# Optimization experiments

Measured on AMD Instinct MI355X. Metric: run time of the kernel, lower is better.

## Reference

```python
import jax, jax.numpy as jnp
import numpy as np

D_MODEL = 1024
N_HEADS = 16
D_K = D_MODEL // N_HEADS


def setup_inputs() -> dict:
    key = jax.random.key(0)
    ks = jax.random.split(key, 9)
    s = 1.0 / np.sqrt(D_MODEL)
    inp = {
        "x": jax.random.normal(ks[0], (2, 2048, D_MODEL), dtype=jnp.float32),
        "wq": jax.random.uniform(ks[1], (D_MODEL, D_MODEL), jnp.float32, -s, s),
        "bq": jax.random.uniform(ks[2], (D_MODEL,), jnp.float32, -s, s),
        "wk": jax.random.uniform(ks[3], (D_MODEL, D_MODEL), jnp.float32, -s, s),
        "bk": jax.random.uniform(ks[4], (D_MODEL,), jnp.float32, -s, s),
        "wv": jax.random.uniform(ks[5], (D_MODEL, D_MODEL), jnp.float32, -s, s),
        "bv": jax.random.uniform(ks[6], (D_MODEL,), jnp.float32, -s, s),
        "wo": jax.random.uniform(ks[7], (D_MODEL, D_MODEL), jnp.float32, -s, s),
        "bo": jax.random.uniform(ks[8], (D_MODEL,), jnp.float32, -s, s),
    }
    return inp


def reference(x, wq, bq, wk, bk, wv, bv, wo, bo):
    B, S, _ = x.shape
    # projections; weights stored as [in, out] (torch Linear applies x @ W^T; here W pre-transposed)
    def proj(w, b):
        y = x @ w + b  # [B,S,D]
        return y.reshape(B, S, N_HEADS, D_K).transpose(0, 2, 1, 3)  # [B,H,S,dk]
    q, k, v = proj(wq, bq), proj(wk, bk), proj(wv, bv)
    scores = jnp.einsum('bhqd,bhkd->bhqk', q, k) / jnp.sqrt(jnp.float32(D_K))
    attn = jax.nn.softmax(scores, axis=-1)  # dropout p=0 -> identity
    ctx = jnp.einsum('bhqk,bhkd->bhqd', attn, v)
    ctx = ctx.transpose(0, 2, 1, 3).reshape(B, S, D_MODEL)
    return ctx @ wo + bo
```

## Files before the change

kernel.cpp:

```cpp
#include <hip/hip_runtime.h>
#include <hip/hip_bf16.h>
#include <math.h>


typedef __attribute__((ext_vector_type(8))) short bf8v;
typedef __attribute__((ext_vector_type(4))) float f32x4;
typedef __attribute__((ext_vector_type(16))) float f32x16;

#define mfma32(a, b, c) __builtin_amdgcn_mfma_f32_32x32x16_bf16((a), (b), (c), 0, 0, 0)

constexpr int Dm = 1024;
constexpr int NH = 16;
constexpr int DK = 64;
constexpr int BB = 2;
constexpr int SS = 2048;
constexpr int MM = BB * SS;

__device__ __forceinline__ unsigned short f2bf(float f) {
  union { float f; unsigned u; } v; v.f = f;
  unsigned r = v.u + 0x7fffu + ((v.u >> 16) & 1u);
  return (unsigned short)(r >> 16);
}

__device__ __forceinline__ unsigned cvt_pk_bf16(float lo, float hi) {
  unsigned r;
  asm("v_cvt_pk_bf16_f32 %0, %1, %2" : "=v"(r) : "v"(lo), "v"(hi));
  return r;
}

__device__ __forceinline__ void swap32(unsigned &a, unsigned &b) {
  asm("v_permlane32_swap_b32 %0, %1" : "+v"(a), "+v"(b));
}

__device__ __forceinline__ void gl_lds16(const void* g, void* l) {
  __builtin_amdgcn_global_load_lds(
      (const __attribute__((address_space(1))) void*)g,
      (__attribute__((address_space(3))) void*)l, 16, 0, 0);
}

__device__ __forceinline__ int swz4(int r) { return (r ^ (r >> 2)) & 3; }
__device__ __forceinline__ bf8v frag4(const unsigned short* base, int R, int s0) {
  return *(const bf8v*)((const char*)base + R * 64 + ((s0 ^ swz4(R)) << 4));
}
__device__ __forceinline__ bf8v rd8(const unsigned short* base, int row, int slot) {
  return *(const bf8v*)((const char*)base + row * 128 + (((slot ^ row) & 7) << 4));
}

__global__ __launch_bounds__(256) void transw_kernel(
    const float* __restrict__ w0, const float* __restrict__ w1,
    const float* __restrict__ w2, const float* __restrict__ w3,
    unsigned short* __restrict__ dstBase)
{
  const float* src = (blockIdx.y == 0) ? w0 : (blockIdx.y == 1) ? w1
                   : (blockIdx.y == 2) ? w2 : w3;
  unsigned short* dst = dstBase + (size_t)blockIdx.y * (Dm * Dm);
  int idx = blockIdx.x * 256 + threadIdx.x;
  int i = idx & (Dm - 1);
  int o = (idx >> 10) << 2;
  float4 v = *(const float4*)(src + (size_t)i * Dm + o);
  dst[(size_t)(o + 0) * Dm + i] = f2bf(v.x);
  dst[(size_t)(o + 1) * Dm + i] = f2bf(v.y);
  dst[(size_t)(o + 2) * Dm + i] = f2bf(v.z);
  dst[(size_t)(o + 3) * Dm + i] = f2bf(v.w);
}

__global__ __launch_bounds__(256) void xconv_kernel(
    const float* __restrict__ x, unsigned short* __restrict__ xb)
{
  int idx = blockIdx.x * 256 + threadIdx.x;
  const float* s = x + (size_t)idx * 8;
  float4 a = *(const float4*)s;
  float4 b = *(const float4*)(s + 4);
  union { bf8v v; unsigned w[4]; } u;
  u.w[0] = cvt_pk_bf16(a.x, a.y); u.w[1] = cvt_pk_bf16(a.z, a.w);
  u.w[2] = cvt_pk_bf16(b.x, b.y); u.w[3] = cvt_pk_bf16(b.z, b.w);
  *(bf8v*)(xb + (size_t)idx * 8) = u.v;
}

__global__ __launch_bounds__(256) void proj_kernel(
    const unsigned short* __restrict__ Xb, const unsigned short* __restrict__ WtBase,
    const float* __restrict__ bq, const float* __restrict__ bk, const float* __restrict__ bv,
    unsigned short* __restrict__ Qh, unsigned short* __restrict__ Kh,
    unsigned short* __restrict__ Vh)
{
  __shared__ unsigned short As[2][128 * 32];
  __shared__ unsigned short Bs[2][128 * 32];
  const int z = blockIdx.z;
  const unsigned short* W = WtBase + (size_t)z * (Dm * Dm);
  const float* bias = (z == 0) ? bq : (z == 1) ? bk : bv;

  const int tid = threadIdx.x, lane = tid & 63, wave = tid >> 6;
  const int wm = wave >> 1, wn = wave & 1;
  const int m0 = blockIdx.x * 128, n0 = blockIdx.y * 128;
  const int l15 = lane & 15, l4 = lane >> 4;

  const int q1 = tid, q2 = tid + 256;
  const int rw1 = q1 >> 2, sl1 = q1 & 3, c1 = sl1 ^ swz4(rw1);
  const int rw2 = q2 >> 2, sl2 = q2 & 3, c2 = sl2 ^ swz4(rw2);
  const int ldsOff1 = (q1 - lane) * 16, ldsOff2 = (q2 - lane) * 16;

  auto stageAB = [&](int buf, int k0) {
    gl_lds16(Xb + (size_t)(m0 + rw1) * Dm + k0 + c1 * 8, (char*)As[buf] + ldsOff1);
    gl_lds16(Xb + (size_t)(m0 + rw2) * Dm + k0 + c2 * 8, (char*)As[buf] + ldsOff2);
    gl_lds16(W + (size_t)(n0 + rw1) * Dm + k0 + c1 * 8, (char*)Bs[buf] + ldsOff1);
    gl_lds16(W + (size_t)(n0 + rw2) * Dm + k0 + c2 * 8, (char*)Bs[buf] + ldsOff2);
  };

  f32x4 acc[4][4] = {};

  stageAB(0, 0);
  __syncthreads();

  for (int k0 = 0; k0 < Dm; k0 += 32) {
    const int cur = (k0 >> 5) & 1, nxt = cur ^ 1;
    if (k0 + 32 < Dm) stageAB(nxt, k0 + 32);

    bf8v af[4], bfr[4];
    #pragma unroll
    for (int i = 0; i < 4; ++i) af[i] = frag4(As[cur], wm * 64 + i * 16 + l15, l4);
    #pragma unroll
    for (int j = 0; j < 4; ++j) bfr[j] = frag4(Bs[cur], wn * 64 + j * 16 + l15, l4);
    __builtin_amdgcn_s_setprio(1);
    #pragma unroll
    for (int i = 0; i < 4; ++i)
      #pragma unroll
      for (int j = 0; j < 4; ++j)
        acc[i][j] = __builtin_amdgcn_mfma_f32_16x16x32_bf16(af[i], bfr[j], acc[i][j], 0, 0, 0);
    __builtin_amdgcn_s_setprio(0);
    __syncthreads();
  }

  unsigned short* Out = (z == 0) ? Qh : (z == 1) ? Kh : Vh;
  const float oscale = (z == 0) ? 0.18033688011112042f : 1.0f;
  #pragma unroll
  for (int i = 0; i < 4; ++i)
    #pragma unroll
    for (int j = 0; j < 4; ++j) {
      int row = m0 + wm * 64 + i * 16 + l4 * 4;
      int col = n0 + wn * 64 + j * 16 + l15;
      float bcol = bias[col];
      int h = col >> 6, d = col & 63;
      #pragma unroll
      for (int r = 0; r < 4; ++r) {
        int rr = row + r;
        int b = rr >> 11, s = rr & 2047;
        unsigned short val = f2bf((acc[i][j][r] + bcol) * oscale);
        if (z < 2)
          Out[(((size_t)(b * NH + h) * SS + s) * DK) + d] = val;
        else
          Out[((size_t)(b * NH + h) * DK + d) * SS + s] = val;
      }
    }
}

__global__ __launch_bounds__(256) void outproj_kernel(
    const unsigned short* __restrict__ Ctx, const unsigned short* __restrict__ Wto,
    const float* __restrict__ bo, float* __restrict__ Out)
{
  __shared__ unsigned short As[2][128 * 32];
  __shared__ unsigned short Bs[2][128 * 32];
  const int tid = threadIdx.x, lane = tid & 63, wave = tid >> 6;
  const int wm = wave >> 1, wn = wave & 1;
  const int m0 = blockIdx.x * 128, n0 = blockIdx.y * 128;
  const int l15 = lane & 15, l4 = lane >> 4;

  const int q1 = tid, q2 = tid + 256;
  const int rw1 = q1 >> 2, sl1 = q1 & 3, c1 = sl1 ^ swz4(rw1);
  const int rw2 = q2 >> 2, sl2 = q2 & 3, c2 = sl2 ^ swz4(rw2);
  const int ldsOff1 = (q1 - lane) * 16, ldsOff2 = (q2 - lane) * 16;

  auto srcA = [&](int rw, int c, int k0) -> const unsigned short* {
    int rr = m0 + rw, b = rr >> 11, s = rr & 2047;
    int col = k0 + c * 8, h = col >> 6, d = col & 63;
    return Ctx + ((size_t)(b * NH + h) * SS + s) * DK + d;
  };
  auto stageAB = [&](int buf, int k0) {
    gl_lds16(srcA(rw1, c1, k0), (char*)As[buf] + ldsOff1);
    gl_lds16(srcA(rw2, c2, k0), (char*)As[buf] + ldsOff2);
    gl_lds16(Wto + (size_t)(n0 + rw1) * Dm + k0 + c1 * 8, (char*)Bs[buf] + ldsOff1);
    gl_lds16(Wto + (size_t)(n0 + rw2) * Dm + k0 + c2 * 8, (char*)Bs[buf] + ldsOff2);
  };

  f32x4 acc[4][4] = {};

  stageAB(0, 0);
  __syncthreads();

  for (int k0 = 0; k0 < Dm; k0 += 32) {
    const int cur = (k0 >> 5) & 1, nxt = cur ^ 1;
    if (k0 + 32 < Dm) stageAB(nxt, k0 + 32);

    bf8v af[4], bfr[4];
    #pragma unroll
    for (int i = 0; i < 4; ++i) af[i] = frag4(As[cur], wm * 64 + i * 16 + l15, l4);
    #pragma unroll
    for (int j = 0; j < 4; ++j) bfr[j] = frag4(Bs[cur], wn * 64 + j * 16 + l15, l4);
    __builtin_amdgcn_s_setprio(1);
    #pragma unroll
    for (int i = 0; i < 4; ++i)
      #pragma unroll
      for (int j = 0; j < 4; ++j)
        acc[i][j] = __builtin_amdgcn_mfma_f32_16x16x32_bf16(af[i], bfr[j], acc[i][j], 0, 0, 0);
    __builtin_amdgcn_s_setprio(0);
    __syncthreads();
  }

  #pragma unroll
  for (int i = 0; i < 4; ++i)
    #pragma unroll
    for (int j = 0; j < 4; ++j) {
      int row = m0 + wm * 64 + i * 16 + l4 * 4;
      int col = n0 + wn * 64 + j * 16 + l15;
      float bcol = bo[col];
      #pragma unroll
      for (int r = 0; r < 4; ++r)
        Out[(size_t)(row + r) * Dm + col] = acc[i][j][r] + bcol;
    }
}

__global__ __launch_bounds__(512, 4) void attn_kernel(
    const unsigned short* __restrict__ Q, const unsigned short* __restrict__ K,
    const unsigned short* __restrict__ Vt, unsigned short* __restrict__ CtxQ)
{
  __shared__ __align__(16) unsigned short smem[32768];
  unsigned short* KlB = smem;
  unsigned short* VlB = smem + 16384;

  const int tid = threadIdx.x, lane = tid & 63, wave = tid >> 6;
  const int qsub = wave & 3, khalf = wave >> 2;
  const int l31 = lane & 31, hi = lane >> 5;
  const int bh = blockIdx.y;
  const int q0 = blockIdx.x * 128 + qsub * 32;
  const size_t base = (size_t)bh * SS * DK;

  bf8v qf[4];
  #pragma unroll
  for (int dc = 0; dc < 4; ++dc)
    qf[dc] = *(const bf8v*)(Q + base + (size_t)(q0 + l31) * DK + dc * 16 + hi * 8);

  bf8v onesv;
  #pragma unroll
  for (int e = 0; e < 8; ++e) onesv[e] = (short)0x3F80;

  f32x16 cacc[2] = {};
  f32x16 lacc = {};

  const int srow = tid >> 3, ssl = tid & 7, sc = ssl ^ (srow & 7);
  const int soff = (tid - lane) * 16;
  auto kslab = [&](int buf, int h) { return KlB + (buf * 2 + h) * 4096; };
  auto vslab = [&](int buf, int h) { return VlB + (buf * 2 + h) * 4096; };
  auto stage = [&](int buf, int kt) {
    gl_lds16(K + base + (size_t)(kt + srow) * DK + sc * 8,          (char*)kslab(buf, 0) + soff);
    gl_lds16(K + base + (size_t)(1024 + kt + srow) * DK + sc * 8,   (char*)kslab(buf, 1) + soff);
    gl_lds16(Vt + base + (size_t)srow * SS + kt + sc * 8,           (char*)vslab(buf, 0) + soff);
    gl_lds16(Vt + base + (size_t)srow * SS + 1024 + kt + sc * 8,    (char*)vslab(buf, 1) + soff);
  };

  constexpr int NT = 16;
  stage(0, 0);
  __syncthreads();

  for (int t = 0; t < NT; ++t) {
    const int cur = t & 1;
    if (t + 1 < NT) stage(cur ^ 1, (t + 1) * 64);
    const unsigned short* Kb = kslab(cur, khalf);
    const unsigned short* Vb = vslab(cur, khalf);

    f32x16 st0 = {}, st1 = {};
    __builtin_amdgcn_s_setprio(1);
    #pragma unroll
    for (int dc = 0; dc < 4; ++dc) {
      bf8v kf0 = rd8(Kb, l31, dc * 2 + hi);
      bf8v kf1 = rd8(Kb, 32 + l31, dc * 2 + hi);
      st0 = mfma32(kf0, qf[dc], st0);
      st1 = mfma32(kf1, qf[dc], st1);
    }
    __builtin_amdgcn_s_setprio(0);

    auto process = [&](const f32x16& st, int ktile) {
      float p[16];
      #pragma unroll
      for (int r = 0; r < 16; ++r) p[r] = exp2f(st[r]);
      #pragma unroll
      for (int c = 0; c < 2; ++c) {
        const int o = c * 8;
        unsigned A  = cvt_pk_bf16(p[o + 0], p[o + 1]);
        unsigned B  = cvt_pk_bf16(p[o + 4], p[o + 5]);
        unsigned Cw = cvt_pk_bf16(p[o + 2], p[o + 3]);
        unsigned Dw = cvt_pk_bf16(p[o + 6], p[o + 7]);
        swap32(A, B); swap32(Cw, Dw);
        union { bf8v v; unsigned w[4]; } pf;
        pf.w[0] = A; pf.w[1] = Cw; pf.w[2] = B; pf.w[3] = Dw;
        const int slot = ktile * 4 + c * 2 + hi;
        bf8v vb0 = rd8(Vb, l31, slot);
        bf8v vb1 = rd8(Vb, 32 + l31, slot);
        __builtin_amdgcn_s_setprio(1);
        cacc[0] = mfma32(vb0, pf.v, cacc[0]);
        cacc[1] = mfma32(vb1, pf.v, cacc[1]);
        lacc    = mfma32(onesv, pf.v, lacc);
        __builtin_amdgcn_s_setprio(0);
      }
    };
    process(st0, 0);
    process(st1, 1);

    __syncthreads();
  }

  float lf = lacc[0];
  float* scr = (float*)smem;
  float* fs = scr + qsub * 2112;

  if (khalf == 1) {
    #pragma unroll
    for (int n = 0; n < 2; ++n)
      #pragma unroll
      for (int r = 0; r < 16; ++r)
        fs[(n * 16 + r) * 64 + lane] = cacc[n][r];
    fs[2048 + lane] = lf;
  }
  __syncthreads();
  if (khalf == 0) {
    float inv = 1.0f / (lf + fs[2048 + lane]);
    #pragma unroll
    for (int n = 0; n < 2; ++n)
      #pragma unroll
      for (int j = 0; j < 4; ++j) {
        float v0 = (cacc[n][4 * j + 0] + fs[(n * 16 + 4 * j + 0) * 64 + lane]) * inv;
        float v1 = (cacc[n][4 * j + 1] + fs[(n * 16 + 4 * j + 1) * 64 + lane]) * inv;
        float v2 = (cacc[n][4 * j + 2] + fs[(n * 16 + 4 * j + 2) * 64 + lane]) * inv;
        float v3 = (cacc[n][4 * j + 3] + fs[(n * 16 + 4 * j + 3) * 64 + lane]) * inv;
        uint2 w;
        w.x = cvt_pk_bf16(v0, v1);
        w.y = cvt_pk_bf16(v2, v3);
        int d = n * 32 + 8 * j + 4 * hi;
        *(uint2*)(CtxQ + base + (size_t)(q0 + l31) * DK + d) = w;
      }
  }
}

extern "C" void kernel_launch(void* const* d_in, const int* in_sizes, int n_in,
                              void* d_out, int out_size, void* d_ws, size_t ws_size,
                              hipStream_t stream) {
  const float* x  = (const float*)d_in[0];
  const float* wq = (const float*)d_in[1];
  const float* bq = (const float*)d_in[2];
  const float* wk = (const float*)d_in[3];
  const float* bk = (const float*)d_in[4];
  const float* wv = (const float*)d_in[5];
  const float* bv = (const float*)d_in[6];
  const float* wo = (const float*)d_in[7];
  const float* bo = (const float*)d_in[8];
  float* out = (float*)d_out;

  unsigned short* ws = (unsigned short*)d_ws;
  const size_t WPLANE = (size_t)Dm * Dm;
  const size_t PLANE  = (size_t)MM * Dm;
  unsigned short* Wt  = ws;
  unsigned short* Qh  = ws + PLANE;
  unsigned short* Kh  = ws + 2 * PLANE;
  unsigned short* Vh  = ws + 3 * PLANE;
  unsigned short* Wto = Wt + 3 * WPLANE;
  unsigned short* Xb  = (unsigned short*)d_out;

  transw_kernel<<<dim3(1024, 4), dim3(256), 0, stream>>>(wq, wk, wv, wo, Wt);
  xconv_kernel<<<dim3(2048), dim3(256), 0, stream>>>(x, Xb);
  proj_kernel<<<dim3(MM / 128, Dm / 128, 3), dim3(256), 0, stream>>>(
      Xb, Wt, bq, bk, bv, Qh, Kh, Vh);
  attn_kernel<<<dim3(SS / 128, BB * NH), dim3(512), 0, stream>>>(Qh, Kh, Vh, Qh);
  outproj_kernel<<<dim3(MM / 128, Dm / 128), dim3(256), 0, stream>>>(Qh, Wto, bo, out);
}
```

Before: 131.7 us.

## Split attention key tiles within a step across waves instead of by key half

The attention kernel shrinks to 256-thread blocks, each covering 64 queries. The 4 waves are split into 2 query subtiles times 2 key halves of each 64-key tile. The two waves in a pair now share one staged 64-key tile per iteration instead of each walking a separate half of the sequence. This halves shared memory per block and doubles the grid, aiming for higher occupancy and better balance. The cost is 32 loop iterations instead of 16, each with less MFMA work per wave, so barrier overhead per unit of work goes up and K/V loads are less reused across query waves.

```diff
diff --git a/kernel.cpp b/kernel.cpp
--- a/kernel.cpp
+++ b/kernel.cpp
@@ -218,19 +218,17 @@
     }
 }
 
-__global__ __launch_bounds__(512, 4) void attn_kernel(
+__global__ __launch_bounds__(256, 4) void attn_kernel(
     const unsigned short* __restrict__ Q, const unsigned short* __restrict__ K,
     const unsigned short* __restrict__ Vt, unsigned short* __restrict__ CtxQ)
 {
-  __shared__ __align__(16) unsigned short smem[32768];
-  unsigned short* KlB = smem;
-  unsigned short* VlB = smem + 16384;
+  __shared__ __align__(16) unsigned short smem[16384];
 
   const int tid = threadIdx.x, lane = tid & 63, wave = tid >> 6;
-  const int qsub = wave & 3, khalf = wave >> 2;
+  const int qsub = wave & 1, ks = wave >> 1;
   const int l31 = lane & 31, hi = lane >> 5;
   const int bh = blockIdx.y;
-  const int q0 = blockIdx.x * 128 + qsub * 32;
+  const int q0 = blockIdx.x * 64 + qsub * 32;
   const size_t base = (size_t)bh * SS * DK;
 
   bf8v qf[4];
@@ -245,64 +243,60 @@
   f32x16 cacc[2] = {};
   f32x16 lacc = {};
 
-  const int srow = tid >> 3, ssl = tid & 7, sc = ssl ^ (srow & 7);
-  const int soff = (tid - lane) * 16;
-  auto kslab = [&](int buf, int h) { return KlB + (buf * 2 + h) * 4096; };
-  auto vslab = [&](int buf, int h) { return VlB + (buf * 2 + h) * 4096; };
+  const int qa = tid, qb = tid + 256;
+  const int rwa = qa >> 3, sla = qa & 7, ca = sla ^ (rwa & 7);
+  const int rwb = qb >> 3, slb = qb & 7, cb = slb ^ (rwb & 7);
+  const int offa = (qa - lane) * 16, offb = (qb - lane) * 16;
+  auto kslab = [&](int buf) { return smem + buf * 4096; };
+  auto vslab = [&](int buf) { return smem + 8192 + buf * 4096; };
   auto stage = [&](int buf, int kt) {
-    gl_lds16(K + base + (size_t)(kt + srow) * DK + sc * 8,          (char*)kslab(buf, 0) + soff);
-    gl_lds16(K + base + (size_t)(1024 + kt + srow) * DK + sc * 8,   (char*)kslab(buf, 1) + soff);
-    gl_lds16(Vt + base + (size_t)srow * SS + kt + sc * 8,           (char*)vslab(buf, 0) + soff);
-    gl_lds16(Vt + base + (size_t)srow * SS + 1024 + kt + sc * 8,    (char*)vslab(buf, 1) + soff);
+    gl_lds16(K + base + (size_t)(kt + rwa) * DK + ca * 8, (char*)kslab(buf) + offa);
+    gl_lds16(K + base + (size_t)(kt + rwb) * DK + cb * 8, (char*)kslab(buf) + offb);
+    gl_lds16(Vt + base + (size_t)rwa * SS + kt + ca * 8,  (char*)vslab(buf) + offa);
+    gl_lds16(Vt + base + (size_t)rwb * SS + kt + cb * 8,  (char*)vslab(buf) + offb);
   };
 
-  constexpr int NT = 16;
+  constexpr int NT = SS / 64;
   stage(0, 0);
   __syncthreads();
 
   for (int t = 0; t < NT; ++t) {
     const int cur = t & 1;
     if (t + 1 < NT) stage(cur ^ 1, (t + 1) * 64);
-    const unsigned short* Kb = kslab(cur, khalf);
-    const unsigned short* Vb = vslab(cur, khalf);
-
-    f32x16 st0 = {}, st1 = {};
+    const unsigned short* Kb = kslab(cur);
+    const unsigned short* Vb = vslab(cur);
+
+    f32x16 st = {};
     __builtin_amdgcn_s_setprio(1);
     #pragma unroll
     for (int dc = 0; dc < 4; ++dc) {
-      bf8v kf0 = rd8(Kb, l31, dc * 2 + hi);
-      bf8v kf1 = rd8(Kb, 32 + l31, dc * 2 + hi);
-      st0 = mfma32(kf0, qf[dc], st0);
-      st1 = mfma32(kf1, qf[dc], st1);
+      bf8v kf = rd8(Kb, ks * 32 + l31, dc * 2 + hi);
+      st = mfma32(kf, qf[dc], st);
     }
     __builtin_amdgcn_s_setprio(0);
 
-    auto process = [&](const f32x16& st, int ktile) {
-      float p[16];
-      #pragma unroll
-      for (int r = 0; r < 16; ++r) p[r] = exp2f(st[r]);
-      #pragma unroll
-      for (int c = 0; c < 2; ++c) {
-        const int o = c * 8;
-        unsigned A  = cvt_pk_bf16(p[o + 0], p[o + 1]);
-        unsigned B  = cvt_pk_bf16(p[o + 4], p[o + 5]);
-        unsigned Cw = cvt_pk_bf16(p[o + 2], p[o + 3]);
-        unsigned Dw = cvt_pk_bf16(p[o + 6], p[o + 7]);
-        swap32(A, B); swap32(Cw, Dw);
-        union { bf8v v; unsigned w[4]; } pf;
-        pf.w[0] = A; pf.w[1] = Cw; pf.w[2] = B; pf.w[3] = Dw;
-        const int slot = ktile * 4 + c * 2 + hi;
-        bf8v vb0 = rd8(Vb, l31, slot);
-        bf8v vb1 = rd8(Vb, 32 + l31, slot);
-        __builtin_amdgcn_s_setprio(1);
-        cacc[0] = mfma32(vb0, pf.v, cacc[0]);
-        cacc[1] = mfma32(vb1, pf.v, cacc[1]);
-        lacc    = mfma32(onesv, pf.v, lacc);
-        __builtin_amdgcn_s_setprio(0);
-      }
-    };
-    process(st0, 0);
-    process(st1, 1);
+    float p[16];
+    #pragma unroll
+    for (int r = 0; r < 16; ++r) p[r] = exp2f(st[r]);
+    #pragma unroll
+    for (int c = 0; c < 2; ++c) {
+      const int o = c * 8;
+      unsigned A  = cvt_pk_bf16(p[o + 0], p[o + 1]);
+      unsigned B  = cvt_pk_bf16(p[o + 4], p[o + 5]);
+      unsigned Cw = cvt_pk_bf16(p[o + 2], p[o + 3]);
+      unsigned Dw = cvt_pk_bf16(p[o + 6], p[o + 7]);
+      swap32(A, B); swap32(Cw, Dw);
+      union { bf8v v; unsigned w[4]; } pf;
+      pf.w[0] = A; pf.w[1] = Cw; pf.w[2] = B; pf.w[3] = Dw;
+      const int slot = ks * 4 + c * 2 + hi;
+      bf8v vb0 = rd8(Vb, l31, slot);
+      bf8v vb1 = rd8(Vb, 32 + l31, slot);
+      __builtin_amdgcn_s_setprio(1);
+      cacc[0] = mfma32(vb0, pf.v, cacc[0]);
+      cacc[1] = mfma32(vb1, pf.v, cacc[1]);
+      lacc    = mfma32(onesv, pf.v, lacc);
+      __builtin_amdgcn_s_setprio(0);
+    }
 
     __syncthreads();
   }
@@ -311,7 +305,7 @@
   float* scr = (float*)smem;
   float* fs = scr + qsub * 2112;
 
-  if (khalf == 1) {
+  if (ks == 1) {
     #pragma unroll
     for (int n = 0; n < 2; ++n)
       #pragma unroll
@@ -320,7 +314,7 @@
     fs[2048 + lane] = lf;
   }
   __syncthreads();
-  if (khalf == 0) {
+  if (ks == 0) {
     float inv = 1.0f / (lf + fs[2048 + lane]);
     #pragma unroll
     for (int n = 0; n < 2; ++n)
@@ -367,6 +361,6 @@
   xconv_kernel<<<dim3(2048), dim3(256), 0, stream>>>(x, Xb);
   proj_kernel<<<dim3(MM / 128, Dm / 128, 3), dim3(256), 0, stream>>>(
       Xb, Wt, bq, bk, bv, Qh, Kh, Vh);
-  attn_kernel<<<dim3(SS / 128, BB * NH), dim3(512), 0, stream>>>(Qh, Kh, Vh, Qh);
+  attn_kernel<<<dim3(SS / 64, BB * NH), dim3(256), 0, stream>>>(Qh, Kh, Vh, Qh);
   outproj_kernel<<<dim3(MM / 128, Dm / 128), dim3(256), 0, stream>>>(Qh, Wto, bo, out);
 }
```

New measurement: 135.0 us. 2.5% more time.
